# Kernel tuning notes

Hardware: AMD Instinct MI355X
Metric: run time of the kernel (lower is better)

Reference implementation:

```python
import jax, jax.numpy as jnp
import numpy as np

N, E, B = 102400, 1638400, 512
DIN, DH, DG = 64, 100, 20
D2, D3 = 200, 300
DF, R, AH, GH, H1, H2, DOUT = 64, 8, 128, 128, 128, 32, 1
EPS = 1e-5


def _xavier(k, i, o):
    lim = float(np.sqrt(6.0 / (i + o)))
    return jax.random.uniform(k, (i, o), minval=-lim, maxval=lim, dtype=jnp.float32)


def setup_inputs() -> dict:
    key = jax.random.key(0)
    ks = jax.random.split(key, 32)
    inp = {
        'node_feat': jax.random.normal(ks[0], (N, DIN), dtype=jnp.float32),
        'self_feat': jax.random.normal(ks[1], (B, D2), dtype=jnp.float32),
        'x3d': jax.random.normal(ks[2], (B, D3), dtype=jnp.float32),
        'src': jax.random.randint(ks[3], (E,), 0, N, dtype=jnp.int32),
        'dst': jax.random.randint(ks[4], (E,), 0, N, dtype=jnp.int32),
        'graph_id': (jnp.arange(N, dtype=jnp.int32) // (N // B)),
        # GCN params (weights stored (in, out))
        'gc1_w': _xavier(ks[5], DIN, DH), 'gc1_b': jnp.zeros((DH,), jnp.float32),
        'gc2_w': _xavier(ks[6], DH, DG), 'gc2_b': jnp.zeros((DG,), jnp.float32),
        # modality gate MLP
        'gate_w1': _xavier(ks[7], DG + D2 + D3, GH), 'gate_b1': jnp.zeros((GH,), jnp.float32),
        'gate_w2': _xavier(ks[8], GH, 3), 'gate_b2': jnp.zeros((3,), jnp.float32),
        # fusion projections + layernorms
        'pg_w': _xavier(ks[9], DG, DF), 'pg_b': jnp.zeros((DF,), jnp.float32),
        'p2_w': _xavier(ks[10], D2, DF), 'p2_b': jnp.zeros((DF,), jnp.float32),
        'p3_w': _xavier(ks[11], D3, DF), 'p3_b': jnp.zeros((DF,), jnp.float32),
        'lng_g': jnp.ones((DF,), jnp.float32), 'lng_b': jnp.zeros((DF,), jnp.float32),
        'ln2_g': jnp.ones((DF,), jnp.float32), 'ln2_b': jnp.zeros((DF,), jnp.float32),
        'ln3_g': jnp.ones((DF,), jnp.float32), 'ln3_b': jnp.zeros((DF,), jnp.float32),
        # low-rank CP factors
        'U_w': _xavier(ks[12], DF, R * DF),
        'V_w': _xavier(ks[13], DF, R * DF),
        'S_w': _xavier(ks[14], DF, R * DF),
        # rank attention MLP
        'attn_w1': _xavier(ks[15], DG + D2 + D3, AH), 'attn_b1': jnp.zeros((AH,), jnp.float32),
        'attn_w2': _xavier(ks[16], AH, R), 'attn_b2': jnp.zeros((R,), jnp.float32),
        # head MLP + batchnorms (training-mode batch stats)
        'fc1_w': _xavier(ks[17], DF, H1), 'fc1_b': jnp.zeros((H1,), jnp.float32),
        'fc2_w': _xavier(ks[18], H1, H2), 'fc2_b': jnp.zeros((H2,), jnp.float32),
        'fc3_w': _xavier(ks[19], H2, DOUT), 'fc3_b': jnp.zeros((DOUT,), jnp.float32),
        'bn1_g': jnp.ones((H1,), jnp.float32), 'bn1_b': jnp.zeros((H1,), jnp.float32),
        'bn2_g': jnp.ones((H2,), jnp.float32), 'bn2_b': jnp.zeros((H2,), jnp.float32),
    }
    return inp


def _gcn(h, src, dst, w, b):
    n = h.shape[0]
    msg = jax.ops.segment_sum(h[src], dst, num_segments=n)           # gather + scatter-add
    deg = jax.ops.segment_sum(jnp.ones((src.shape[0],), h.dtype), dst, num_segments=n)
    agg = msg / jnp.maximum(deg, 1.0)[:, None]                       # mean over mailbox
    return agg @ w + b


def _ln(x, g, b):
    mu = jnp.mean(x, axis=-1, keepdims=True)
    var = jnp.mean(jnp.square(x - mu), axis=-1, keepdims=True)
    return g * (x - mu) * jax.lax.rsqrt(var + EPS) + b


def _bn(x, g, b):
    mu = jnp.mean(x, axis=0)
    var = jnp.mean(jnp.square(x - mu), axis=0)
    return g * (x - mu) * jax.lax.rsqrt(var + EPS) + b


def reference(node_feat, self_feat, x3d, src, dst, graph_id,
              gc1_w, gc1_b, gc2_w, gc2_b,
              gate_w1, gate_b1, gate_w2, gate_b2,
              pg_w, pg_b, p2_w, p2_b, p3_w, p3_b,
              lng_g, lng_b, ln2_g, ln2_b, ln3_g, ln3_b,
              U_w, V_w, S_w,
              attn_w1, attn_b1, attn_w2, attn_b2,
              fc1_w, fc1_b, fc2_w, fc2_b, fc3_w, fc3_b,
              bn1_g, bn1_b, bn2_g, bn2_b):
    b = self_feat.shape[0]
    # two GCN layers (copy_u + mean reduce + linear), relu
    h = jax.nn.relu(_gcn(node_feat, src, dst, gc1_w, gc1_b))
    h = jax.nn.relu(_gcn(h, src, dst, gc2_w, gc2_b))
    # dgl.mean_nodes: per-graph mean readout
    cnt = jax.ops.segment_sum(jnp.ones((h.shape[0],), h.dtype), graph_id, num_segments=b)
    hg = jax.ops.segment_sum(h, graph_id, num_segments=b) / cnt[:, None]  # (B, DG)
    # modality gate
    cat = jnp.concatenate([hg, self_feat, x3d], axis=-1)
    alpha = jax.nn.softmax(jax.nn.relu(cat @ gate_w1 + gate_b1) @ gate_w2 + gate_b2, axis=-1)
    hg2 = hg * alpha[:, 0:1]
    sf2 = self_feat * alpha[:, 1:2]
    x3d2 = x3d * alpha[:, 2:3]
    # low-rank tri-linear fusion with rank attention (dropout = identity, eval mode)
    gp = jax.nn.relu(_ln(hg2 @ pg_w + pg_b, lng_g, lng_b))
    d2 = jax.nn.relu(_ln(sf2 @ p2_w + p2_b, ln2_g, ln2_b))
    d3 = jax.nn.relu(_ln(x3d2 @ p3_w + p3_b, ln3_g, ln3_b))
    g_r = (gp @ U_w).reshape(b, R, DF)
    d2_r = (d2 @ V_w).reshape(b, R, DF)
    d3_r = (d3 @ S_w).reshape(b, R, DF)
    z_r = g_r * d2_r * d3_r                                          # (B, R, DF)
    cat2 = jnp.concatenate([hg2, sf2, x3d2], axis=-1)
    beta = jax.nn.softmax(jax.nn.relu(cat2 @ attn_w1 + attn_b1) @ attn_w2 + attn_b2, axis=-1)
    z = jnp.sum(z_r * beta[:, :, None], axis=1)                      # (B, DF)
    # head MLP with batchnorm (batch statistics)
    out = jax.nn.relu(_bn(z @ fc1_w + fc1_b, bn1_g, bn1_b))
    out = jax.nn.relu(_bn(out @ fc2_w + fc2_b, bn2_g, bn2_b))
    out = out @ fc3_w + fc3_b
    return out
```

## Files before the change

### kernel.cpp

```cpp
#include <hip/hip_runtime.h>

#define N_NODES 102400
#define N_EDGES 1638400
#define BB 512
#define DIN 64
#define DH 100
#define DG 20
#define D2 200
#define D3 300
#define DF 64
#define RR 8
#define H1 128
#define H2 32
#define NPG (N_NODES / BB)
#define EPSV 1e-5f
#define CAP 48
#define TB6 6
#define NSLICE 8
#define SLICEN (N_NODES / NSLICE)

typedef float v2f __attribute__((ext_vector_type(2)));

__device__ __forceinline__ float wave_sum64(float v) {
#pragma unroll
    for (int m = 32; m >= 1; m >>= 1) v += __shfl_xor(v, m, 64);
    return v;
}

__device__ __forceinline__ unsigned enc4_fp8(float x0, float x1, float x2, float x3) {
    int r = __builtin_amdgcn_cvt_pk_fp8_f32(x0, x1, 0, false);
    r = __builtin_amdgcn_cvt_pk_fp8_f32(x2, x3, r, true);
    return (unsigned)r;
}
__device__ __forceinline__ void dec8_acc(uint2 w, float* a) {
    v2f p0 = __builtin_amdgcn_cvt_pk_f32_fp8((int)w.x, false);
    v2f p1 = __builtin_amdgcn_cvt_pk_f32_fp8((int)w.x, true);
    v2f p2 = __builtin_amdgcn_cvt_pk_f32_fp8((int)w.y, false);
    v2f p3 = __builtin_amdgcn_cvt_pk_f32_fp8((int)w.y, true);
    a[0] += p0.x; a[1] += p0.y; a[2] += p1.x; a[3] += p1.y;
    a[4] += p2.x; a[5] += p2.y; a[6] += p3.x; a[7] += p3.y;
}

__global__ __launch_bounds__(256) void prep(
    const float* __restrict__ nf, unsigned* __restrict__ nfb,
    const int* __restrict__ src, const int* __restrict__ dst,
    int* __restrict__ counts, int* __restrict__ col) {
    int b = blockIdx.x, t = threadIdx.x;
    if (b < 6400) {
        int i = b * 256 + t;
        float4 v = ((const float4*)nf)[i];
        nfb[i] = enc4_fp8(v.x, v.y, v.z, v.w);
    } else {
        int idx = b - 6400;
        int slice = idx & 7;
        int chunk = idx >> 3;
        int e = chunk * 256 + t;
        int d = dst[e];
        if ((d / SLICEN) == slice) {
            int pos = atomicAdd(&counts[d], 1);
            if (pos < CAP) col[d * CAP + pos] = src[e];
        }
    }
}

__global__ __launch_bounds__(512) void gcn1_gather(
    const unsigned* __restrict__ nfb, const int* __restrict__ counts,
    const int* __restrict__ col,
    const float* __restrict__ w1, const float* __restrict__ b1,
    const float* __restrict__ w2, unsigned* __restrict__ tb) {
    __shared__ float s_in[8][DIN];
    __shared__ float s_h[8][DH];
    const uint2* nfb2 = (const uint2*)nfb;
    int t = threadIdx.x;
    int wid = t >> 6, l = t & 63;
    int o = l & 7;
    int g = l >> 3;
    int n0 = blockIdx.x * 8;
    int n = n0 + wid;
    int cnt = counts[n]; if (cnt > CAP) cnt = CAP;
    float a[8];
#pragma unroll
    for (int j = 0; j < 8; j++) a[j] = 0.f;
    int idx = (l < cnt) ? col[n * CAP + l] : 0;
    int nIter = cnt >> 3;
    int m = 0;
    for (; m + 3 < nIter; m += 4) {
        int s0 = __shfl(idx, (m + 0) * 8 + g, 64);
        int s1 = __shfl(idx, (m + 1) * 8 + g, 64);
        int s2 = __shfl(idx, (m + 2) * 8 + g, 64);
        int s3 = __shfl(idx, (m + 3) * 8 + g, 64);
        uint2 v0 = nfb2[(size_t)s0 * 8 + o];
        uint2 v1 = nfb2[(size_t)s1 * 8 + o];
        uint2 v2 = nfb2[(size_t)s2 * 8 + o];
        uint2 v3 = nfb2[(size_t)s3 * 8 + o];
        dec8_acc(v0, a); dec8_acc(v1, a); dec8_acc(v2, a); dec8_acc(v3, a);
    }
    for (; m + 1 < nIter; m += 2) {
        int s0 = __shfl(idx, (m + 0) * 8 + g, 64);
        int s1 = __shfl(idx, (m + 1) * 8 + g, 64);
        uint2 v0 = nfb2[(size_t)s0 * 8 + o];
        uint2 v1 = nfb2[(size_t)s1 * 8 + o];
        dec8_acc(v0, a); dec8_acc(v1, a);
    }
    if (m < nIter) {
        int s0 = __shfl(idx, m * 8 + g, 64);
        uint2 v0 = nfb2[(size_t)s0 * 8 + o];
        dec8_acc(v0, a);
    }
    int base = nIter << 3;
    if (base < cnt) {
        int kt = base + g;
        int kl = (kt < cnt) ? kt : (cnt - 1);
        int s = __shfl(idx, kl, 64);
        if (kt < cnt) {
            uint2 v0 = nfb2[(size_t)s * 8 + o];
            dec8_acc(v0, a);
        }
    }
#pragma unroll
    for (int mm = 8; mm <= 32; mm <<= 1) {
#pragma unroll
        for (int j = 0; j < 8; j++) a[j] += __shfl_xor(a[j], mm, 64);
    }
    if (l < 8) {
        float dv = fmaxf((float)cnt, 1.0f);
#pragma unroll
        for (int j = 0; j < 8; j++) s_in[wid][8 * l + j] = a[j] / dv;
    }
    __syncthreads();
    if (t < 400) {
        int j = t / 100;
        int c = t % 100;
        float bv = b1[c];
        float accA = bv, accB = bv;
        for (int i = 0; i < DIN; i++) {
            float w = w1[i * DH + c];
            accA += s_in[j][i] * w;
            accB += s_in[j + 4][i] * w;
        }
        s_h[j][c] = fmaxf(accA, 0.f);
        s_h[j + 4][c] = fmaxf(accB, 0.f);
    }
    __syncthreads();
    if (t < 8 * TB6) {
        int j = t / TB6, p = t % TB6;
        unsigned pk = 0u;
        if (p < 5) {
            float x[4];
#pragma unroll
            for (int q = 0; q < 4; q++) x[q] = 0.f;
            for (int i = 0; i < DH; i++) {
                float hv = s_h[j][i];
#pragma unroll
                for (int q = 0; q < 4; q++) x[q] += hv * w2[i * DG + 4 * p + q];
            }
            pk = enc4_fp8(x[0], x[1], x[2], x[3]);
        }
        tb[(size_t)(n0 + j) * TB6 + p] = pk;
    }
}

__global__ __launch_bounds__(512) void gcn2_gather(
    const unsigned* __restrict__ tb, const int* __restrict__ counts,
    const int* __restrict__ col,
    const float* __restrict__ b2, float* __restrict__ hg) {
    const uint2* tb2 = (const uint2*)tb;
    int t = threadIdx.x;
    int wid = t >> 6, l = t & 63;
    int o = l & 3;
    int g = l >> 2;
    int n = blockIdx.x * 8 + wid;
    int cnt = counts[n]; if (cnt > CAP) cnt = CAP;
    float a[8];
#pragma unroll
    for (int j = 0; j < 8; j++) a[j] = 0.f;
    int idx = (l < cnt) ? col[n * CAP + l] : 0;
    int nIter = cnt >> 4;
    int m = 0;
    for (; m + 1 < nIter; m += 2) {
        int sA = __shfl(idx, (m + 0) * 16 + g, 64);
        int sB = __shfl(idx, (m + 1) * 16 + g, 64);
        uint2 vA = make_uint2(0u, 0u);
        uint2 vB = make_uint2(0u, 0u);
        if (o < 3) { vA = tb2[(size_t)sA * 3 + o]; vB = tb2[(size_t)sB * 3 + o]; }
        dec8_acc(vA, a); dec8_acc(vB, a);
    }
    if (m < nIter) {
        int s = __shfl(idx, m * 16 + g, 64);
        uint2 v = make_uint2(0u, 0u);
        if (o < 3) v = tb2[(size_t)s * 3 + o];
        dec8_acc(v, a);
    }
    int base = nIter << 4;
    if (base < cnt) {
        int kt = base + g;
        int kl = (kt < cnt) ? kt : (cnt - 1);
        int s = __shfl(idx, kl, 64);
        if (kt < cnt && o < 3) {
            uint2 v = tb2[(size_t)s * 3 + o];
            dec8_acc(v, a);
        }
    }
#pragma unroll
    for (int mm = 4; mm <= 32; mm <<= 1) {
#pragma unroll
        for (int j = 0; j < 8; j++) a[j] += __shfl_xor(a[j], mm, 64);
    }
    __shared__ float red[8][DG];
    if (l < 3) {
        float dv = fmaxf((float)cnt, 1.0f);
#pragma unroll
        for (int j = 0; j < 8; j++) {
            int f = 8 * l + j;
            if (f < DG) red[wid][f] = fmaxf(a[j] / dv + b2[f], 0.f);
        }
    }
    __syncthreads();
    if (t < DG) {
        float s = 0.f;
#pragma unroll
        for (int j = 0; j < 8; j++) s += red[j][t];
        atomicAdd(&hg[(blockIdx.x / 25) * DG + t], s * (1.0f / (float)NPG));
    }
}

__device__ __forceinline__ float ln_relu(float x, float g, float b) {
    float mu = wave_sum64(x) * (1.0f / DF);
    float d = x - mu;
    float var = wave_sum64(d * d) * (1.0f / DF);
    float v = g * d * rsqrtf(var + EPSV) + b;
    return fmaxf(v, 0.f);
}

__global__ __launch_bounds__(512) void row_tail(
    const float* __restrict__ hg, const float* __restrict__ sf, const float* __restrict__ x3,
    const float* __restrict__ gate_w1, const float* __restrict__ gate_b1,
    const float* __restrict__ gate_w2, const float* __restrict__ gate_b2,
    const float* __restrict__ attn_w1, const float* __restrict__ attn_b1,
    const float* __restrict__ attn_w2, const float* __restrict__ attn_b2,
    const float* __restrict__ pg_w, const float* __restrict__ pg_b,
    const float* __restrict__ p2_w, const float* __restrict__ p2_b,
    const float* __restrict__ p3_w, const float* __restrict__ p3_b,
    const float* __restrict__ lng_g, const float* __restrict__ lng_b,
    const float* __restrict__ ln2_g, const float* __restrict__ ln2_b,
    const float* __restrict__ ln3_g, const float* __restrict__ ln3_b,
    const float* __restrict__ U_w, const float* __restrict__ V_w, const float* __restrict__ S_w,
    const float* __restrict__ fc1_w, const float* __restrict__ fc1_b,
    float* __restrict__ y1) {
    int row = blockIdx.x, t = threadIdx.x;
    __shared__ float s_in[DG + D2 + D3];
    __shared__ float s_part[512];
    __shared__ float s_hid[128];
    __shared__ float s_sm[RR];
    __shared__ float s_alpha[3];
    __shared__ float s_beta[RR];
    __shared__ float s_gp[DF], s_d2[DF], s_d3[DF], s_z[DF];

    for (int i = t; i < DG + D2 + D3; i += 512)
        s_in[i] = (i < DG) ? hg[row * DG + i]
                : (i < DG + D2) ? sf[row * D2 + (i - DG)]
                : x3[row * D3 + (i - DG - D2)];
    __syncthreads();

    {
        int ks = t >> 7, col = t & 127;
        int k0 = ks * 130;
        float acc = 0.f;
        for (int i = k0; i < k0 + 130; i++) acc += s_in[i] * gate_w1[i * 128 + col];
        s_part[ks * 128 + col] = acc;
    }
    __syncthreads();
    if (t < 128)
        s_hid[t] = fmaxf(s_part[t] + s_part[128 + t] + s_part[256 + t] + s_part[384 + t]
                         + gate_b1[t], 0.f);
    __syncthreads();
    if (t < 3) {
        float p = gate_b2[t];
        for (int i = 0; i < 128; i++) p += s_hid[i] * gate_w2[i * 3 + t];
        s_sm[t] = p;
    }
    __syncthreads();
    if (t == 0) {
        float mx = fmaxf(s_sm[0], fmaxf(s_sm[1], s_sm[2]));
        float e0 = __expf(s_sm[0] - mx), e1 = __expf(s_sm[1] - mx), e2 = __expf(s_sm[2] - mx);
        float inv = 1.0f / (e0 + e1 + e2);
        s_alpha[0] = e0 * inv; s_alpha[1] = e1 * inv; s_alpha[2] = e2 * inv;
    }
    __syncthreads();
    for (int i = t; i < DG + D2 + D3; i += 512) {
        float sc = (i < DG) ? s_alpha[0] : (i < DG + D2) ? s_alpha[1] : s_alpha[2];
        s_in[i] *= sc;
    }
    __syncthreads();

    {
        int ks = t >> 7, col = t & 127;
        int k0 = ks * 130;
        float acc = 0.f;
        for (int i = k0; i < k0 + 130; i++) acc += s_in[i] * attn_w1[i * 128 + col];
        s_part[ks * 128 + col] = acc;
    }
    __syncthreads();
    if (t < 128)
        s_hid[t] = fmaxf(s_part[t] + s_part[128 + t] + s_part[256 + t] + s_part[384 + t]
                         + attn_b1[t], 0.f);
    __syncthreads();
    if (t < RR) {
        float p = attn_b2[t];
        for (int i = 0; i < 128; i++) p += s_hid[i] * attn_w2[i * RR + t];
        s_sm[t] = p;
    }
    __syncthreads();
    if (t == 0) {
        float mx = -1e30f;
#pragma unroll
        for (int k = 0; k < RR; k++) mx = fmaxf(mx, s_sm[k]);
        float se = 0.f, e[RR];
#pragma unroll
        for (int k = 0; k < RR; k++) { e[k] = __expf(s_sm[k] - mx); se += e[k]; }
        float inv = 1.0f / se;
#pragma unroll
        for (int k = 0; k < RR; k++) s_beta[k] = e[k] * inv;
    }
    __syncthreads();

    float rawg = 0.f, raw2 = 0.f, raw3 = 0.f;
    if (t < DF) {
        rawg = pg_b[t];
        for (int i = 0; i < DG; i++) rawg += s_in[i] * pg_w[i * DF + t];
    }
    {
        int ks = t >> 6, col = t & 63;
        int k0 = ks * 25;
        float acc = 0.f;
        for (int u = 0; u < 25; u++) acc += s_in[DG + k0 + u] * p2_w[(k0 + u) * DF + col];
        s_part[ks * 64 + col] = acc;
    }
    __syncthreads();
    if (t < DF) {
        raw2 = p2_b[t];
#pragma unroll
        for (int r = 0; r < 8; r++) raw2 += s_part[r * 64 + t];
    }
    __syncthreads();
    {
        int ks = t >> 6, col = t & 63;
        int k0 = (ks * 300) >> 3, k1 = ((ks + 1) * 300) >> 3;
        float acc = 0.f;
        for (int i = k0; i < k1; i++) acc += s_in[DG + D2 + i] * p3_w[i * DF + col];
        s_part[ks * 64 + col] = acc;
    }
    __syncthreads();
    if (t < DF) {
        raw3 = p3_b[t];
#pragma unroll
        for (int r = 0; r < 8; r++) raw3 += s_part[r * 64 + t];
        s_gp[t] = ln_relu(rawg, lng_g[t], lng_b[t]);
        s_d2[t] = ln_relu(raw2, ln2_g[t], ln2_b[t]);
        s_d3[t] = ln_relu(raw3, ln3_g[t], ln3_b[t]);
    }
    __syncthreads();

    {
        int r = t >> 6, f = t & 63;
        float gu = 0.f, dv = 0.f, ds = 0.f;
        for (int i = 0; i < DF; i++) {
            gu += s_gp[i] * U_w[i * (RR * DF) + r * DF + f];
            dv += s_d2[i] * V_w[i * (RR * DF) + r * DF + f];
            ds += s_d3[i] * S_w[i * (RR * DF) + r * DF + f];
        }
        s_part[r * 64 + f] = s_beta[r] * gu * dv * ds;
    }
    __syncthreads();
    if (t < DF) {
        float zf = 0.f;
#pragma unroll
        for (int r = 0; r < RR; r++) zf += s_part[r * 64 + t];
        s_z[t] = zf;
    }
    __syncthreads();

    {
        int ks = t >> 7, col = t & 127;
        int k0 = ks * 16;
        float acc = 0.f;
        for (int i = k0; i < k0 + 16; i++) acc += s_z[i] * fc1_w[i * H1 + col];
        s_part[ks * 128 + col] = acc;
    }
    __syncthreads();
    if (t < 128)
        y1[row * H1 + t] = s_part[t] + s_part[128 + t] + s_part[256 + t] + s_part[384 + t]
                           + fc1_b[t];
}

__global__ __launch_bounds__(256) void head2(
    const float* __restrict__ y1,
    const float* __restrict__ bn1_g, const float* __restrict__ bn1_b,
    const float* __restrict__ fc2_w, const float* __restrict__ fc2_b,
    float* __restrict__ y2) {
    int row = blockIdx.x, t = threadIdx.x;
    __shared__ float sp[2][H1], sp2[2][H1];
    int h = t >> 7, c = t & 127;
    float s = 0.f, s2 = 0.f;
#pragma unroll 8
    for (int r = h * 256; r < h * 256 + 256; r++) {
        float v = y1[r * H1 + c];
        s += v; s2 += v * v;
    }
    sp[h][c] = s; sp2[h][c] = s2;
    __syncthreads();
    __shared__ float sh[H1];
    if (t < H1) {
        float S = sp[0][t] + sp[1][t];
        float S2 = sp2[0][t] + sp2[1][t];
        float m = S * (1.0f / BB);
        float ri = rsqrtf(S2 * (1.0f / BB) - m * m + EPSV);
        float v = y1[row * H1 + t];
        sh[t] = fmaxf(bn1_g[t] * (v - m) * ri + bn1_b[t], 0.f);
    }
    __syncthreads();
    if (t < H2) {
        float acc = fc2_b[t];
        for (int i = 0; i < H1; i++) acc += sh[i] * fc2_w[i * H2 + t];
        y2[row * H2 + t] = acc;
    }
}

__global__ __launch_bounds__(256) void head3(
    const float* __restrict__ y2,
    const float* __restrict__ bn2_g, const float* __restrict__ bn2_b,
    const float* __restrict__ fc3_w, const float* __restrict__ fc3_b,
    float* __restrict__ out) {
    int t = threadIdx.x;
    __shared__ float smu[H2], sri[H2];
    if (t < H2) {
        float s = 0.f, s2 = 0.f;
#pragma unroll 8
        for (int r = 0; r < BB; r++) {
            float v = y2[r * H2 + t];
            s += v; s2 += v * v;
        }
        float m = s * (1.0f / BB);
        smu[t] = m;
        sri[t] = rsqrtf(s2 * (1.0f / BB) - m * m + EPSV);
    }
    __syncthreads();
    int row = blockIdx.x * 256 + t;
    float acc = fc3_b[0];
    for (int i = 0; i < H2; i++) {
        float v = y2[row * H2 + i];
        v = bn2_g[i] * (v - smu[i]) * sri[i] + bn2_b[i];
        acc += fmaxf(v, 0.f) * fc3_w[i];
    }
    out[row] = acc;
}

extern "C" void kernel_launch(void* const* d_in, const int* in_sizes, int n_in,
                              void* d_out, int out_size, void* d_ws, size_t ws_size,
                              hipStream_t stream) {
    const float* node_feat = (const float*)d_in[0];
    const float* self_feat = (const float*)d_in[1];
    const float* x3d       = (const float*)d_in[2];
    const int*   src       = (const int*)d_in[3];
    const int*   dst       = (const int*)d_in[4];
    const float* gc1_w = (const float*)d_in[6];
    const float* gc1_b = (const float*)d_in[7];
    const float* gc2_w = (const float*)d_in[8];
    const float* gc2_b = (const float*)d_in[9];
    const float* gate_w1 = (const float*)d_in[10];
    const float* gate_b1 = (const float*)d_in[11];
    const float* gate_w2 = (const float*)d_in[12];
    const float* gate_b2 = (const float*)d_in[13];
    const float* pg_w = (const float*)d_in[14];
    const float* pg_b = (const float*)d_in[15];
    const float* p2_w = (const float*)d_in[16];
    const float* p2_b = (const float*)d_in[17];
    const float* p3_w = (const float*)d_in[18];
    const float* p3_b = (const float*)d_in[19];
    const float* lng_g = (const float*)d_in[20];
    const float* lng_b = (const float*)d_in[21];
    const float* ln2_g = (const float*)d_in[22];
    const float* ln2_b = (const float*)d_in[23];
    const float* ln3_g = (const float*)d_in[24];
    const float* ln3_b = (const float*)d_in[25];
    const float* U_w = (const float*)d_in[26];
    const float* V_w = (const float*)d_in[27];
    const float* S_w = (const float*)d_in[28];
    const float* attn_w1 = (const float*)d_in[29];
    const float* attn_b1 = (const float*)d_in[30];
    const float* attn_w2 = (const float*)d_in[31];
    const float* attn_b2 = (const float*)d_in[32];
    const float* fc1_w = (const float*)d_in[33];
    const float* fc1_b = (const float*)d_in[34];
    const float* fc2_w = (const float*)d_in[35];
    const float* fc2_b = (const float*)d_in[36];
    const float* fc3_w = (const float*)d_in[37];
    const float* fc3_b = (const float*)d_in[38];
    const float* bn1_g = (const float*)d_in[39];
    const float* bn1_b = (const float*)d_in[40];
    const float* bn2_g = (const float*)d_in[41];
    const float* bn2_b = (const float*)d_in[42];

    char* base = (char*)d_ws;
    int* counts  = (int*)base;                       base += sizeof(int) * N_NODES;
    int* col     = (int*)base;                       base += sizeof(int) * (size_t)N_NODES * CAP;
    unsigned* nfb = (unsigned*)base;                 base += sizeof(unsigned) * (size_t)N_NODES * 16;
    unsigned* tb  = (unsigned*)base;                 base += sizeof(unsigned) * (size_t)N_NODES * TB6;
    float* hg    = (float*)base;                     base += sizeof(float) * BB * DG;
    float* y1    = (float*)base;                     base += sizeof(float) * BB * H1;
    float* y2    = (float*)base;                     base += sizeof(float) * BB * H2;
    float* outf  = (float*)d_out;

    hipMemsetAsync(counts, 0, sizeof(int) * N_NODES, stream);
    hipMemsetAsync(hg, 0, sizeof(float) * BB * DG, stream);

    prep<<<6400 + 51200, 256, 0, stream>>>(node_feat, nfb, src, dst, counts, col);

    gcn1_gather<<<N_NODES / 8, 512, 0, stream>>>(nfb, counts, col,
                                                 gc1_w, gc1_b, gc2_w, tb);
    gcn2_gather<<<N_NODES / 8, 512, 0, stream>>>(tb, counts, col, gc2_b, hg);

    row_tail<<<BB, 512, 0, stream>>>(hg, self_feat, x3d,
                                     gate_w1, gate_b1, gate_w2, gate_b2,
                                     attn_w1, attn_b1, attn_w2, attn_b2,
                                     pg_w, pg_b, p2_w, p2_b, p3_w, p3_b,
                                     lng_g, lng_b, ln2_g, ln2_b, ln3_g, ln3_b,
                                     U_w, V_w, S_w, fc1_w, fc1_b, y1);
    head2<<<BB, 256, 0, stream>>>(y1, bn1_g, bn1_b, fc2_w, fc2_b, y2);
    head3<<<BB / 256, 256, 0, stream>>>(y2, bn2_g, bn2_b, fc3_w, fc3_b, outf);
}
```

Measured before the change: 453.8 us.

## Apply GCN layer-1 weight before aggregation and gather projected fp8 rows

Node features are now multiplied by the first GCN weight in the prep kernel, using linearity to reorder mean-aggregation and the matmul. The 100-wide result is stored as fp8 in 104-byte rows, and gcn1_gather gathers these instead of 64-byte raw rows. This drops the per-block 64x100 matmul after aggregation. In exchange the gather moves about 1.6x more bytes per edge, and fp8 rounding now happens after projection rather than before. Accumulation also switches to packed 2-float vector adds in both gather kernels.

```diff
diff --git a/kernel.cpp b/kernel.cpp
--- a/kernel.cpp
+++ b/kernel.cpp
@@ -16,6 +16,7 @@
 #define EPSV 1e-5f
 #define CAP 48
 #define TB6 6
+#define TQ6 26
 #define NSLICE 8
 #define SLICEN (N_NODES / NSLICE)
 
@@ -32,24 +33,39 @@
     r = __builtin_amdgcn_cvt_pk_fp8_f32(x2, x3, r, true);
     return (unsigned)r;
 }
-__device__ __forceinline__ void dec8_acc(uint2 w, float* a) {
-    v2f p0 = __builtin_amdgcn_cvt_pk_f32_fp8((int)w.x, false);
-    v2f p1 = __builtin_amdgcn_cvt_pk_f32_fp8((int)w.x, true);
-    v2f p2 = __builtin_amdgcn_cvt_pk_f32_fp8((int)w.y, false);
-    v2f p3 = __builtin_amdgcn_cvt_pk_f32_fp8((int)w.y, true);
-    a[0] += p0.x; a[1] += p0.y; a[2] += p1.x; a[3] += p1.y;
-    a[4] += p2.x; a[5] += p2.y; a[6] += p3.x; a[7] += p3.y;
+__device__ __forceinline__ void dec8_acc2(uint2 w, v2f* a) {
+    a[0] += __builtin_amdgcn_cvt_pk_f32_fp8((int)w.x, false);
+    a[1] += __builtin_amdgcn_cvt_pk_f32_fp8((int)w.x, true);
+    a[2] += __builtin_amdgcn_cvt_pk_f32_fp8((int)w.y, false);
+    a[3] += __builtin_amdgcn_cvt_pk_f32_fp8((int)w.y, true);
 }
 
 __global__ __launch_bounds__(256) void prep(
-    const float* __restrict__ nf, unsigned* __restrict__ nfb,
+    const float* __restrict__ nf, const float* __restrict__ w1,
+    unsigned* __restrict__ Tq,
     const int* __restrict__ src, const int* __restrict__ dst,
     int* __restrict__ counts, int* __restrict__ col) {
+    __shared__ float s_nf[16][65];
     int b = blockIdx.x, t = threadIdx.x;
     if (b < 6400) {
-        int i = b * 256 + t;
-        float4 v = ((const float4*)nf)[i];
-        nfb[i] = enc4_fp8(v.x, v.y, v.z, v.w);
+        int n0 = b * 16;
+        float4 v = ((const float4*)nf)[b * 256 + t];
+        int row = t >> 4, c4 = (t & 15) * 4;
+        s_nf[row][c4] = v.x; s_nf[row][c4 + 1] = v.y;
+        s_nf[row][c4 + 2] = v.z; s_nf[row][c4 + 3] = v.w;
+        __syncthreads();
+        for (int task = t; task < 400; task += 256) {
+            int nn = task / 25, p = task % 25;
+            float a0 = 0.f, a1 = 0.f, a2 = 0.f, a3 = 0.f;
+#pragma unroll 8
+            for (int i = 0; i < DIN; i++) {
+                float x = s_nf[nn][i];
+                float4 w = *(const float4*)&w1[i * DH + 4 * p];
+                a0 += x * w.x; a1 += x * w.y; a2 += x * w.z; a3 += x * w.w;
+            }
+            Tq[(size_t)(n0 + nn) * TQ6 + p] = enc4_fp8(a0, a1, a2, a3);
+        }
+        if (t < 16) Tq[(size_t)(n0 + t) * TQ6 + 25] = 0u;
     } else {
         int idx = b - 6400;
         int slice = idx & 7;
@@ -64,98 +80,96 @@
 }
 
 __global__ __launch_bounds__(512) void gcn1_gather(
-    const unsigned* __restrict__ nfb, const int* __restrict__ counts,
+    const unsigned* __restrict__ Tq, const int* __restrict__ counts,
     const int* __restrict__ col,
-    const float* __restrict__ w1, const float* __restrict__ b1,
-    const float* __restrict__ w2, unsigned* __restrict__ tb) {
-    __shared__ float s_in[8][DIN];
-    __shared__ float s_h[8][DH];
-    const uint2* nfb2 = (const uint2*)nfb;
+    const float* __restrict__ b1, const float* __restrict__ w2,
+    unsigned* __restrict__ tb) {
+    __shared__ float s_h[8][104];
+    __shared__ float s_o[8][DG];
+    const uint2* T2 = (const uint2*)Tq;
     int t = threadIdx.x;
     int wid = t >> 6, l = t & 63;
-    int o = l & 7;
-    int g = l >> 3;
+    int o = l & 15;
+    int g = l >> 4;
     int n0 = blockIdx.x * 8;
     int n = n0 + wid;
     int cnt = counts[n]; if (cnt > CAP) cnt = CAP;
-    float a[8];
-#pragma unroll
-    for (int j = 0; j < 8; j++) a[j] = 0.f;
+    bool ok = (o < 13);
+    uint2 zz = make_uint2(0u, 0u);
+    v2f a2[4];
+#pragma unroll
+    for (int j = 0; j < 4; j++) { a2[j].x = 0.f; a2[j].y = 0.f; }
     int idx = (l < cnt) ? col[n * CAP + l] : 0;
-    int nIter = cnt >> 3;
+    int nIter = cnt >> 2;
     int m = 0;
     for (; m + 3 < nIter; m += 4) {
-        int s0 = __shfl(idx, (m + 0) * 8 + g, 64);
-        int s1 = __shfl(idx, (m + 1) * 8 + g, 64);
-        int s2 = __shfl(idx, (m + 2) * 8 + g, 64);
-        int s3 = __shfl(idx, (m + 3) * 8 + g, 64);
-        uint2 v0 = nfb2[(size_t)s0 * 8 + o];
-        uint2 v1 = nfb2[(size_t)s1 * 8 + o];
-        uint2 v2 = nfb2[(size_t)s2 * 8 + o];
-        uint2 v3 = nfb2[(size_t)s3 * 8 + o];
-        dec8_acc(v0, a); dec8_acc(v1, a); dec8_acc(v2, a); dec8_acc(v3, a);
+        int s0 = __shfl(idx, (m + 0) * 4 + g, 64);
+        int s1 = __shfl(idx, (m + 1) * 4 + g, 64);
+        int s2 = __shfl(idx, (m + 2) * 4 + g, 64);
+        int s3 = __shfl(idx, (m + 3) * 4 + g, 64);
+        uint2 v0 = ok ? T2[(size_t)s0 * 13 + o] : zz;
+        uint2 v1 = ok ? T2[(size_t)s1 * 13 + o] : zz;
+        uint2 v2 = ok ? T2[(size_t)s2 * 13 + o] : zz;
+        uint2 v3 = ok ? T2[(size_t)s3 * 13 + o] : zz;
+        dec8_acc2(v0, a2); dec8_acc2(v1, a2); dec8_acc2(v2, a2); dec8_acc2(v3, a2);
     }
     for (; m + 1 < nIter; m += 2) {
-        int s0 = __shfl(idx, (m + 0) * 8 + g, 64);
-        int s1 = __shfl(idx, (m + 1) * 8 + g, 64);
-        uint2 v0 = nfb2[(size_t)s0 * 8 + o];
-        uint2 v1 = nfb2[(size_t)s1 * 8 + o];
-        dec8_acc(v0, a); dec8_acc(v1, a);
+        int s0 = __shfl(idx, (m + 0) * 4 + g, 64);
+        int s1 = __shfl(idx, (m + 1) * 4 + g, 64);
+        uint2 v0 = ok ? T2[(size_t)s0 * 13 + o] : zz;
+        uint2 v1 = ok ? T2[(size_t)s1 * 13 + o] : zz;
+        dec8_acc2(v0, a2); dec8_acc2(v1, a2);
     }
     if (m < nIter) {
-        int s0 = __shfl(idx, m * 8 + g, 64);
-        uint2 v0 = nfb2[(size_t)s0 * 8 + o];
-        dec8_acc(v0, a);
-    }
-    int base = nIter << 3;
+        int s0 = __shfl(idx, m * 4 + g, 64);
+        uint2 v0 = ok ? T2[(size_t)s0 * 13 + o] : zz;
+        dec8_acc2(v0, a2);
+    }
+    int base = nIter << 2;
     if (base < cnt) {
         int kt = base + g;
         int kl = (kt < cnt) ? kt : (cnt - 1);
         int s = __shfl(idx, kl, 64);
-        if (kt < cnt) {
-            uint2 v0 = nfb2[(size_t)s * 8 + o];
-            dec8_acc(v0, a);
-        }
-    }
-#pragma unroll
-    for (int mm = 8; mm <= 32; mm <<= 1) {
-#pragma unroll
-        for (int j = 0; j < 8; j++) a[j] += __shfl_xor(a[j], mm, 64);
-    }
-    if (l < 8) {
-        float dv = fmaxf((float)cnt, 1.0f);
-#pragma unroll
-        for (int j = 0; j < 8; j++) s_in[wid][8 * l + j] = a[j] / dv;
-    }
-    __syncthreads();
-    if (t < 400) {
-        int j = t / 100;
-        int c = t % 100;
-        float bv = b1[c];
-        float accA = bv, accB = bv;
-        for (int i = 0; i < DIN; i++) {
-            float w = w1[i * DH + c];
-            accA += s_in[j][i] * w;
-            accB += s_in[j + 4][i] * w;
-        }
-        s_h[j][c] = fmaxf(accA, 0.f);
-        s_h[j + 4][c] = fmaxf(accB, 0.f);
+        if (kt < cnt && ok) {
+            uint2 v0 = T2[(size_t)s * 13 + o];
+            dec8_acc2(v0, a2);
+        }
+    }
+#pragma unroll
+    for (int mm = 16; mm <= 32; mm <<= 1) {
+#pragma unroll
+        for (int j = 0; j < 4; j++) {
+            v2f oth;
+            oth.x = __shfl_xor(a2[j].x, mm, 64);
+            oth.y = __shfl_xor(a2[j].y, mm, 64);
+            a2[j] += oth;
+        }
+    }
+    if (l < 13) {
+        float inv = 1.0f / fmaxf((float)cnt, 1.0f);
+        float av[8] = {a2[0].x, a2[0].y, a2[1].x, a2[1].y,
+                       a2[2].x, a2[2].y, a2[3].x, a2[3].y};
+#pragma unroll
+        for (int j = 0; j < 8; j++) {
+            int f = 8 * l + j;
+            if (f < DH) s_h[wid][f] = fmaxf(av[j] * inv + b1[f], 0.f);
+        }
+    }
+    __syncthreads();
+    if (t < 160) {
+        int j = t / 20, c = t % 20;
+        float acc = 0.f;
+#pragma unroll 4
+        for (int i = 0; i < DH; i++) acc += s_h[j][i] * w2[i * DG + c];
+        s_o[j][c] = acc;
     }
     __syncthreads();
     if (t < 8 * TB6) {
         int j = t / TB6, p = t % TB6;
         unsigned pk = 0u;
-        if (p < 5) {
-            float x[4];
-#pragma unroll
-            for (int q = 0; q < 4; q++) x[q] = 0.f;
-            for (int i = 0; i < DH; i++) {
-                float hv = s_h[j][i];
-#pragma unroll
-                for (int q = 0; q < 4; q++) x[q] += hv * w2[i * DG + 4 * p + q];
-            }
-            pk = enc4_fp8(x[0], x[1], x[2], x[3]);
-        }
+        if (p < 5)
+            pk = enc4_fp8(s_o[j][4 * p], s_o[j][4 * p + 1],
+                          s_o[j][4 * p + 2], s_o[j][4 * p + 3]);
         tb[(size_t)(n0 + j) * TB6 + p] = pk;
     }
 }
@@ -171,48 +185,55 @@
     int g = l >> 2;
     int n = blockIdx.x * 8 + wid;
     int cnt = counts[n]; if (cnt > CAP) cnt = CAP;
-    float a[8];
-#pragma unroll
-    for (int j = 0; j < 8; j++) a[j] = 0.f;
+    bool ok = (o < 3);
+    uint2 zz = make_uint2(0u, 0u);
+    v2f a2[4];
+#pragma unroll
+    for (int j = 0; j < 4; j++) { a2[j].x = 0.f; a2[j].y = 0.f; }
     int idx = (l < cnt) ? col[n * CAP + l] : 0;
     int nIter = cnt >> 4;
     int m = 0;
     for (; m + 1 < nIter; m += 2) {
         int sA = __shfl(idx, (m + 0) * 16 + g, 64);
         int sB = __shfl(idx, (m + 1) * 16 + g, 64);
-        uint2 vA = make_uint2(0u, 0u);
-        uint2 vB = make_uint2(0u, 0u);
-        if (o < 3) { vA = tb2[(size_t)sA * 3 + o]; vB = tb2[(size_t)sB * 3 + o]; }
-        dec8_acc(vA, a); dec8_acc(vB, a);
+        uint2 vA = ok ? tb2[(size_t)sA * 3 + o] : zz;
+        uint2 vB = ok ? tb2[(size_t)sB * 3 + o] : zz;
+        dec8_acc2(vA, a2); dec8_acc2(vB, a2);
     }
     if (m < nIter) {
         int s = __shfl(idx, m * 16 + g, 64);
-        uint2 v = make_uint2(0u, 0u);
-        if (o < 3) v = tb2[(size_t)s * 3 + o];
-        dec8_acc(v, a);
+        uint2 v = ok ? tb2[(size_t)s * 3 + o] : zz;
+        dec8_acc2(v, a2);
     }
     int base = nIter << 4;
     if (base < cnt) {
         int kt = base + g;
         int kl = (kt < cnt) ? kt : (cnt - 1);
         int s = __shfl(idx, kl, 64);
-        if (kt < cnt && o < 3) {
+        if (kt < cnt && ok) {
             uint2 v = tb2[(size_t)s * 3 + o];
-            dec8_acc(v, a);
+            dec8_acc2(v, a2);
         }
     }
 #pragma unroll
     for (int mm = 4; mm <= 32; mm <<= 1) {
 #pragma unroll
-        for (int j = 0; j < 8; j++) a[j] += __shfl_xor(a[j], mm, 64);
+        for (int j = 0; j < 4; j++) {
+            v2f oth;
+            oth.x = __shfl_xor(a2[j].x, mm, 64);
+            oth.y = __shfl_xor(a2[j].y, mm, 64);
+            a2[j] += oth;
+        }
     }
     __shared__ float red[8][DG];
     if (l < 3) {
-        float dv = fmaxf((float)cnt, 1.0f);
+        float inv = 1.0f / fmaxf((float)cnt, 1.0f);
+        float av[8] = {a2[0].x, a2[0].y, a2[1].x, a2[1].y,
+                       a2[2].x, a2[2].y, a2[3].x, a2[3].y};
 #pragma unroll
         for (int j = 0; j < 8; j++) {
             int f = 8 * l + j;
-            if (f < DG) red[wid][f] = fmaxf(a[j] / dv + b2[f], 0.f);
+            if (f < DG) red[wid][f] = fmaxf(av[j] * inv + b2[f], 0.f);
         }
     }
     __syncthreads();
@@ -504,7 +525,7 @@
     char* base = (char*)d_ws;
     int* counts  = (int*)base;                       base += sizeof(int) * N_NODES;
     int* col     = (int*)base;                       base += sizeof(int) * (size_t)N_NODES * CAP;
-    unsigned* nfb = (unsigned*)base;                 base += sizeof(unsigned) * (size_t)N_NODES * 16;
+    unsigned* Tq  = (unsigned*)base;                 base += sizeof(unsigned) * (size_t)N_NODES * TQ6;
     unsigned* tb  = (unsigned*)base;                 base += sizeof(unsigned) * (size_t)N_NODES * TB6;
     float* hg    = (float*)base;                     base += sizeof(float) * BB * DG;
     float* y1    = (float*)base;                     base += sizeof(float) * BB * H1;
@@ -514,10 +535,9 @@
     hipMemsetAsync(counts, 0, sizeof(int) * N_NODES, stream);
     hipMemsetAsync(hg, 0, sizeof(float) * BB * DG, stream);
 
-    prep<<<6400 + 51200, 256, 0, stream>>>(node_feat, nfb, src, dst, counts, col);
-
-    gcn1_gather<<<N_NODES / 8, 512, 0, stream>>>(nfb, counts, col,
-                                                 gc1_w, gc1_b, gc2_w, tb);
+    prep<<<6400 + 51200, 256, 0, stream>>>(node_feat, gc1_w, Tq, src, dst, counts, col);
+
+    gcn1_gather<<<N_NODES / 8, 512, 0, stream>>>(Tq, counts, col, gc1_b, gc2_w, tb);
     gcn2_gather<<<N_NODES / 8, 512, 0, stream>>>(tb, counts, col, gc2_b, hg);
 
     row_tail<<<BB, 512, 0, stream>>>(hg, self_feat, x3d,
```

After: 545.4 us. 20.2% more time.

## Split GCN layer-1 gather from dense transforms into separate tiled kernel

Applied to the files above, without the earlier changes.

Layer-1 is split in two. One kernel now only gathers and averages neighbours and writes bf16 aggregates. A second kernel runs the W1/ReLU/W2 matmuls over 64-node tiles with register-blocked accumulators. This frees the gather from low-utilisation matmul phases with idle threads and improves weight reuse, at the cost of an extra launch and a round trip of bf16 intermediates through memory. The gathers also accumulate in packed float2, use nontemporal loads for the column indices, and multiply by a reciprocal instead of dividing.

```diff
diff --git a/kernel.cpp b/kernel.cpp
--- a/kernel.cpp
+++ b/kernel.cpp
@@ -32,13 +32,19 @@
     r = __builtin_amdgcn_cvt_pk_fp8_f32(x2, x3, r, true);
     return (unsigned)r;
 }
-__device__ __forceinline__ void dec8_acc(uint2 w, float* a) {
-    v2f p0 = __builtin_amdgcn_cvt_pk_f32_fp8((int)w.x, false);
-    v2f p1 = __builtin_amdgcn_cvt_pk_f32_fp8((int)w.x, true);
-    v2f p2 = __builtin_amdgcn_cvt_pk_f32_fp8((int)w.y, false);
-    v2f p3 = __builtin_amdgcn_cvt_pk_f32_fp8((int)w.y, true);
-    a[0] += p0.x; a[1] += p0.y; a[2] += p1.x; a[3] += p1.y;
-    a[4] += p2.x; a[5] += p2.y; a[6] += p3.x; a[7] += p3.y;
+__device__ __forceinline__ void dec8_acc2(uint2 w, v2f* a) {
+    a[0] += __builtin_amdgcn_cvt_pk_f32_fp8((int)w.x, false);
+    a[1] += __builtin_amdgcn_cvt_pk_f32_fp8((int)w.x, true);
+    a[2] += __builtin_amdgcn_cvt_pk_f32_fp8((int)w.y, false);
+    a[3] += __builtin_amdgcn_cvt_pk_f32_fp8((int)w.y, true);
+}
+__device__ __forceinline__ unsigned short f2bf(float x) {
+    unsigned u = __float_as_uint(x);
+    u += 0x7fffu + ((u >> 16) & 1u);
+    return (unsigned short)(u >> 16);
+}
+__device__ __forceinline__ float bf2f(unsigned u16) {
+    return __uint_as_float(u16 << 16);
 }
 
 __global__ __launch_bounds__(256) void prep(
@@ -63,25 +69,20 @@
     }
 }
 
-__global__ __launch_bounds__(512) void gcn1_gather(
+__global__ __launch_bounds__(512) void agg_gather(
     const unsigned* __restrict__ nfb, const int* __restrict__ counts,
-    const int* __restrict__ col,
-    const float* __restrict__ w1, const float* __restrict__ b1,
-    const float* __restrict__ w2, unsigned* __restrict__ tb) {
-    __shared__ float s_in[8][DIN];
-    __shared__ float s_h[8][DH];
+    const int* __restrict__ col, unsigned short* __restrict__ aggb) {
     const uint2* nfb2 = (const uint2*)nfb;
     int t = threadIdx.x;
     int wid = t >> 6, l = t & 63;
     int o = l & 7;
     int g = l >> 3;
-    int n0 = blockIdx.x * 8;
-    int n = n0 + wid;
+    int n = blockIdx.x * 8 + wid;
     int cnt = counts[n]; if (cnt > CAP) cnt = CAP;
-    float a[8];
-#pragma unroll
-    for (int j = 0; j < 8; j++) a[j] = 0.f;
-    int idx = (l < cnt) ? col[n * CAP + l] : 0;
+    v2f a2[4];
+#pragma unroll
+    for (int j = 0; j < 4; j++) { a2[j].x = 0.f; a2[j].y = 0.f; }
+    int idx = (l < cnt) ? __builtin_nontemporal_load(&col[n * CAP + l]) : 0;
     int nIter = cnt >> 3;
     int m = 0;
     for (; m + 3 < nIter; m += 4) {
@@ -93,19 +94,19 @@
         uint2 v1 = nfb2[(size_t)s1 * 8 + o];
         uint2 v2 = nfb2[(size_t)s2 * 8 + o];
         uint2 v3 = nfb2[(size_t)s3 * 8 + o];
-        dec8_acc(v0, a); dec8_acc(v1, a); dec8_acc(v2, a); dec8_acc(v3, a);
+        dec8_acc2(v0, a2); dec8_acc2(v1, a2); dec8_acc2(v2, a2); dec8_acc2(v3, a2);
     }
     for (; m + 1 < nIter; m += 2) {
         int s0 = __shfl(idx, (m + 0) * 8 + g, 64);
         int s1 = __shfl(idx, (m + 1) * 8 + g, 64);
         uint2 v0 = nfb2[(size_t)s0 * 8 + o];
         uint2 v1 = nfb2[(size_t)s1 * 8 + o];
-        dec8_acc(v0, a); dec8_acc(v1, a);
+        dec8_acc2(v0, a2); dec8_acc2(v1, a2);
     }
     if (m < nIter) {
         int s0 = __shfl(idx, m * 8 + g, 64);
         uint2 v0 = nfb2[(size_t)s0 * 8 + o];
-        dec8_acc(v0, a);
+        dec8_acc2(v0, a2);
     }
     int base = nIter << 3;
     if (base < cnt) {
@@ -114,50 +115,86 @@
         int s = __shfl(idx, kl, 64);
         if (kt < cnt) {
             uint2 v0 = nfb2[(size_t)s * 8 + o];
-            dec8_acc(v0, a);
+            dec8_acc2(v0, a2);
         }
     }
 #pragma unroll
     for (int mm = 8; mm <= 32; mm <<= 1) {
 #pragma unroll
-        for (int j = 0; j < 8; j++) a[j] += __shfl_xor(a[j], mm, 64);
+        for (int j = 0; j < 4; j++) {
+            v2f oth;
+            oth.x = __shfl_xor(a2[j].x, mm, 64);
+            oth.y = __shfl_xor(a2[j].y, mm, 64);
+            a2[j] += oth;
+        }
     }
     if (l < 8) {
-        float dv = fmaxf((float)cnt, 1.0f);
-#pragma unroll
-        for (int j = 0; j < 8; j++) s_in[wid][8 * l + j] = a[j] / dv;
-    }
-    __syncthreads();
-    if (t < 400) {
-        int j = t / 100;
-        int c = t % 100;
-        float bv = b1[c];
-        float accA = bv, accB = bv;
+        float inv = 1.0f / fmaxf((float)cnt, 1.0f);
+        float av[8] = {a2[0].x, a2[0].y, a2[1].x, a2[1].y,
+                       a2[2].x, a2[2].y, a2[3].x, a2[3].y};
+        unsigned us[8];
+#pragma unroll
+        for (int j = 0; j < 8; j++) us[j] = (unsigned)f2bf(av[j] * inv);
+        uint4 w;
+        w.x = us[0] | (us[1] << 16);
+        w.y = us[2] | (us[3] << 16);
+        w.z = us[4] | (us[5] << 16);
+        w.w = us[6] | (us[7] << 16);
+        *(uint4*)(aggb + (size_t)n * 64 + 8 * l) = w;
+    }
+}
+
+__global__ __launch_bounds__(256) void w12(
+    const unsigned short* __restrict__ aggb,
+    const float* __restrict__ w1, const float* __restrict__ b1,
+    const float* __restrict__ w2, unsigned* __restrict__ tb) {
+    __shared__ float s_a[64][65];
+    __shared__ float s_h[64][101];
+    int b = blockIdx.x, t = threadIdx.x;
+    int n0 = b * 64;
+    const uint4* ag4 = (const uint4*)(aggb + (size_t)n0 * 64);
+#pragma unroll
+    for (int k = 0; k < 2; k++) {
+        int q = t + k * 256;
+        uint4 w = ag4[q];
+        int row = q >> 3, c8 = (q & 7) * 8;
+        s_a[row][c8 + 0] = bf2f(w.x & 0xffffu);
+        s_a[row][c8 + 1] = bf2f(w.x >> 16);
+        s_a[row][c8 + 2] = bf2f(w.y & 0xffffu);
+        s_a[row][c8 + 3] = bf2f(w.y >> 16);
+        s_a[row][c8 + 4] = bf2f(w.z & 0xffffu);
+        s_a[row][c8 + 5] = bf2f(w.z >> 16);
+        s_a[row][c8 + 6] = bf2f(w.w & 0xffffu);
+        s_a[row][c8 + 7] = bf2f(w.w >> 16);
+    }
+    __syncthreads();
+    {
+        int j = t >> 2;
+        int c0 = (t & 3) * 25;
+        float acc[25];
+#pragma unroll
+        for (int cc = 0; cc < 25; cc++) acc[cc] = b1[c0 + cc];
         for (int i = 0; i < DIN; i++) {
-            float w = w1[i * DH + c];
-            accA += s_in[j][i] * w;
-            accB += s_in[j + 4][i] * w;
-        }
-        s_h[j][c] = fmaxf(accA, 0.f);
-        s_h[j + 4][c] = fmaxf(accB, 0.f);
-    }
-    __syncthreads();
-    if (t < 8 * TB6) {
-        int j = t / TB6, p = t % TB6;
-        unsigned pk = 0u;
-        if (p < 5) {
-            float x[4];
-#pragma unroll
-            for (int q = 0; q < 4; q++) x[q] = 0.f;
-            for (int i = 0; i < DH; i++) {
-                float hv = s_h[j][i];
-#pragma unroll
-                for (int q = 0; q < 4; q++) x[q] += hv * w2[i * DG + 4 * p + q];
-            }
-            pk = enc4_fp8(x[0], x[1], x[2], x[3]);
-        }
-        tb[(size_t)(n0 + j) * TB6 + p] = pk;
-    }
+            float x = s_a[j][i];
+            const float* wr = &w1[i * DH + c0];
+#pragma unroll
+            for (int cc = 0; cc < 25; cc++) acc[cc] += x * wr[cc];
+        }
+#pragma unroll
+        for (int cc = 0; cc < 25; cc++) s_h[j][c0 + cc] = fmaxf(acc[cc], 0.f);
+    }
+    __syncthreads();
+    for (int task = t; task < 320; task += 256) {
+        int j = task / 5, p = task % 5;
+        float a0 = 0.f, a1 = 0.f, a2 = 0.f, a3 = 0.f;
+        for (int i = 0; i < DH; i++) {
+            float hv = s_h[j][i];
+            float4 w = *(const float4*)&w2[i * DG + 4 * p];
+            a0 += hv * w.x; a1 += hv * w.y; a2 += hv * w.z; a3 += hv * w.w;
+        }
+        tb[(size_t)(n0 + j) * TB6 + p] = enc4_fp8(a0, a1, a2, a3);
+    }
+    if (t < 64) tb[(size_t)(n0 + t) * TB6 + 5] = 0u;
 }
 
 __global__ __launch_bounds__(512) void gcn2_gather(
@@ -171,48 +208,55 @@
     int g = l >> 2;
     int n = blockIdx.x * 8 + wid;
     int cnt = counts[n]; if (cnt > CAP) cnt = CAP;
-    float a[8];
-#pragma unroll
-    for (int j = 0; j < 8; j++) a[j] = 0.f;
-    int idx = (l < cnt) ? col[n * CAP + l] : 0;
+    bool ok = (o < 3);
+    uint2 zz = make_uint2(0u, 0u);
+    v2f a2[4];
+#pragma unroll
+    for (int j = 0; j < 4; j++) { a2[j].x = 0.f; a2[j].y = 0.f; }
+    int idx = (l < cnt) ? __builtin_nontemporal_load(&col[n * CAP + l]) : 0;
     int nIter = cnt >> 4;
     int m = 0;
     for (; m + 1 < nIter; m += 2) {
         int sA = __shfl(idx, (m + 0) * 16 + g, 64);
         int sB = __shfl(idx, (m + 1) * 16 + g, 64);
-        uint2 vA = make_uint2(0u, 0u);
-        uint2 vB = make_uint2(0u, 0u);
-        if (o < 3) { vA = tb2[(size_t)sA * 3 + o]; vB = tb2[(size_t)sB * 3 + o]; }
-        dec8_acc(vA, a); dec8_acc(vB, a);
+        uint2 vA = ok ? tb2[(size_t)sA * 3 + o] : zz;
+        uint2 vB = ok ? tb2[(size_t)sB * 3 + o] : zz;
+        dec8_acc2(vA, a2); dec8_acc2(vB, a2);
     }
     if (m < nIter) {
         int s = __shfl(idx, m * 16 + g, 64);
-        uint2 v = make_uint2(0u, 0u);
-        if (o < 3) v = tb2[(size_t)s * 3 + o];
-        dec8_acc(v, a);
+        uint2 v = ok ? tb2[(size_t)s * 3 + o] : zz;
+        dec8_acc2(v, a2);
     }
     int base = nIter << 4;
     if (base < cnt) {
         int kt = base + g;
         int kl = (kt < cnt) ? kt : (cnt - 1);
         int s = __shfl(idx, kl, 64);
-        if (kt < cnt && o < 3) {
+        if (kt < cnt && ok) {
             uint2 v = tb2[(size_t)s * 3 + o];
-            dec8_acc(v, a);
+            dec8_acc2(v, a2);
         }
     }
 #pragma unroll
     for (int mm = 4; mm <= 32; mm <<= 1) {
 #pragma unroll
-        for (int j = 0; j < 8; j++) a[j] += __shfl_xor(a[j], mm, 64);
+        for (int j = 0; j < 4; j++) {
+            v2f oth;
+            oth.x = __shfl_xor(a2[j].x, mm, 64);
+            oth.y = __shfl_xor(a2[j].y, mm, 64);
+            a2[j] += oth;
+        }
     }
     __shared__ float red[8][DG];
     if (l < 3) {
-        float dv = fmaxf((float)cnt, 1.0f);
+        float inv = 1.0f / fmaxf((float)cnt, 1.0f);
+        float av[8] = {a2[0].x, a2[0].y, a2[1].x, a2[1].y,
+                       a2[2].x, a2[2].y, a2[3].x, a2[3].y};
 #pragma unroll
         for (int j = 0; j < 8; j++) {
             int f = 8 * l + j;
-            if (f < DG) red[wid][f] = fmaxf(a[j] / dv + b2[f], 0.f);
+            if (f < DG) red[wid][f] = fmaxf(av[j] * inv + b2[f], 0.f);
         }
     }
     __syncthreads();
@@ -506,6 +550,7 @@
     int* col     = (int*)base;                       base += sizeof(int) * (size_t)N_NODES * CAP;
     unsigned* nfb = (unsigned*)base;                 base += sizeof(unsigned) * (size_t)N_NODES * 16;
     unsigned* tb  = (unsigned*)base;                 base += sizeof(unsigned) * (size_t)N_NODES * TB6;
+    unsigned short* aggb = (unsigned short*)base;    base += sizeof(unsigned short) * (size_t)N_NODES * 64;
     float* hg    = (float*)base;                     base += sizeof(float) * BB * DG;
     float* y1    = (float*)base;                     base += sizeof(float) * BB * H1;
     float* y2    = (float*)base;                     base += sizeof(float) * BB * H2;
@@ -516,8 +561,8 @@
 
     prep<<<6400 + 51200, 256, 0, stream>>>(node_feat, nfb, src, dst, counts, col);
 
-    gcn1_gather<<<N_NODES / 8, 512, 0, stream>>>(nfb, counts, col,
-                                                 gc1_w, gc1_b, gc2_w, tb);
+    agg_gather<<<N_NODES / 8, 512, 0, stream>>>(nfb, counts, col, aggb);
+    w12<<<N_NODES / 64, 256, 0, stream>>>(aggb, gc1_w, gc1_b, gc2_w, tb);
     gcn2_gather<<<N_NODES / 8, 512, 0, stream>>>(tb, counts, col, gc2_b, hg);
 
     row_tail<<<BB, 512, 0, stream>>>(hg, self_feat, x3d,
```

After: 537.8 us. 1.19x slower.
